# Kernel tuning notes

Hardware: AMD Instinct MI355X
Metric: run time of the kernel (lower is better)

The kernel has to match this reference:

```python
import jax, jax.numpy as jnp
import numpy as np

B, HQ, HKV, D = 32, 32, 8, 128
PAGE_SIZE, PAGES_PER_SEQ = 16, 128
NUM_PAGES = B * PAGES_PER_SEQ
MAX_LEN = PAGE_SIZE * PAGES_PER_SEQ  # 2048
SCALING = 0.08838834764831845  # 1/sqrt(128)
LOGIT_CAP = 50.0


def setup_inputs() -> dict:
    key = jax.random.key(0)
    ks = jax.random.split(key, 6)
    q = jax.random.normal(ks[0], (B, HQ * D), jnp.float32)
    k = jax.random.normal(ks[1], (B, HKV * D), jnp.float32)
    v = jax.random.normal(ks[2], (B, HKV * D), jnp.float32)
    k_cache = jax.random.normal(ks[3], (NUM_PAGES, PAGE_SIZE, HKV, D), jnp.float32)
    v_cache = jax.random.normal(ks[4], (NUM_PAGES, PAGE_SIZE, HKV, D), jnp.float32)
    # disjoint page assignment: request b owns pages [b*128, (b+1)*128)
    page_table = jnp.arange(NUM_PAGES, dtype=jnp.int32).reshape(B, PAGES_PER_SEQ)
    seq_lens = jax.random.randint(ks[5], (B,), 1, MAX_LEN + 1, dtype=jnp.int32)
    return dict(q=q, k=k, v=v, k_cache=k_cache, v_cache=v_cache,
                page_table=page_table, seq_lens=seq_lens)


def reference(q, k, v, k_cache, v_cache, page_table, seq_lens):
    # mirror RadixAttention.forward's k.view(-1, Hkv, D) / v.view(-1, Hkv, D)
    kn = k.reshape(B, HKV, D)
    vn = v.reshape(B, HKV, D)

    # save_kv_cache=True: scatter new token (at position seq_len-1) into paged cache
    pos = seq_lens - 1
    page = page_table[jnp.arange(B), pos // PAGE_SIZE]  # [B]
    slot = pos % PAGE_SIZE                              # [B]
    k_cache = k_cache.at[page, slot].set(kn)
    v_cache = v_cache.at[page, slot].set(vn)

    # gather paged KV per request: [B, Lmax, Hkv, D]
    Kb = k_cache[page_table].reshape(B, MAX_LEN, HKV, D)
    Vb = v_cache[page_table].reshape(B, MAX_LEN, HKV, D)

    # GQA: query head h maps to kv head h // (HQ//HKV)
    G = HQ // HKV
    qh = q.reshape(B, HKV, G, D)
    scores = jnp.einsum('bkgd,blkd->bkgl', qh, Kb) * SCALING  # [B,Hkv,G,L]
    scores = LOGIT_CAP * jnp.tanh(scores / LOGIT_CAP)          # logit capping

    valid = jnp.arange(MAX_LEN, dtype=jnp.int32)[None, :] < seq_lens[:, None]  # [B,L]
    scores = jnp.where(valid[:, None, None, :], scores, -jnp.inf)
    p = jax.nn.softmax(scores, axis=-1)
    out = jnp.einsum('bkgl,blkd->bkgd', p, Vb)  # [B,Hkv,G,D]
    return out.reshape(B, HQ * D)
```

## Files before the change

### kernel.cpp

```cpp
#include <hip/hip_runtime.h>
#include <hip/hip_bf16.h>
#include <math.h>

#define BB 32
#define HQ 32
#define HKV 8
#define DD 128
#define PAGE_SZ 16
#define PAGES_PER_SEQ 128
#define MAX_LEN 2048
#define GG 4
#define NCHUNK 8
#define CHUNK 256
#define SCALING 0.08838834764831845f
#define CAP 50.0f
#define WS_STRIDE 520

__global__ __launch_bounds__(256, 4) void attn_partial(
    const float* __restrict__ q,
    const float* __restrict__ knew,
    const float* __restrict__ vnew,
    const float* __restrict__ k_cache,
    const float* __restrict__ v_cache,
    const int* __restrict__ page_table,
    const int* __restrict__ seq_lens,
    float* __restrict__ ws)
{
    const int idx = blockIdx.x;
    const int c  = idx % NCHUNK;
    const int bh = idx / NCHUNK;
    const int h  = bh % HKV;
    const int b  = bh / HKV;

    const int L  = seq_lens[b];
    const int t0 = c * CHUNK;
    const int t1 = min(t0 + CHUNK, L);
    float* wsb = ws + (size_t)idx * WS_STRIDE;

    if (t0 >= t1) {
        if (threadIdx.x < GG) { wsb[threadIdx.x] = -INFINITY; wsb[GG + threadIdx.x] = 0.0f; }
        return;
    }
    const int NT = t1 - t0;

    __shared__ float s_q[GG][DD];
    __shared__ float s_sc[GG][CHUNK];
    __shared__ float s_red[8][GG * DD];
    __shared__ int   s_pages[CHUNK / PAGE_SZ];
    __shared__ float s_m[GG], s_l[GG];

    const int tid = threadIdx.x;

    for (int i = tid; i < GG * DD; i += 256) {
        int g = i / DD, d = i % DD;
        s_q[g][d] = q[(size_t)b * (HQ * DD) + (h * GG + g) * DD + d];
    }
    if (tid < CHUNK / PAGE_SZ)
        s_pages[tid] = page_table[b * PAGES_PER_SEQ + t0 / PAGE_SZ + tid];
    __syncthreads();

    const int hw = tid >> 5;
    const int ln = tid & 31;

    float4 qf[GG];
    #pragma unroll
    for (int g = 0; g < GG; g++) qf[g] = *(const float4*)&s_q[g][4 * ln];

    const float4* knew_row = (const float4*)&knew[(size_t)b * (HKV * DD) + h * DD];
    const float4* vnew_row = (const float4*)&vnew[(size_t)b * (HKV * DD) + h * DD];

    for (int i = 0; i < CHUNK / 32; i++) {
        const int tbase = t0 + i * 32 + hw;
        if (tbase >= t1) break;

        float4 kv[4];
        int   trel[4];
        bool  vld[4];
        #pragma unroll
        for (int j = 0; j < 4; j++) {
            int t = tbase + j * 8;
            vld[j] = (t < t1);
            int tc = vld[j] ? t : tbase;
            trel[j] = tc - t0;
            const float4* krow;
            if (tc == L - 1) {
                krow = knew_row;
            } else {
                int page = s_pages[trel[j] >> 4];
                int slot = tc & (PAGE_SZ - 1);
                krow = (const float4*)&k_cache[((size_t)page * PAGE_SZ + slot) * (HKV * DD) + h * DD];
            }
            kv[j] = krow[ln];
        }

        float dots[4][GG];
        #pragma unroll
        for (int j = 0; j < 4; j++) {
            #pragma unroll
            for (int g = 0; g < GG; g++)
                dots[j][g] = kv[j].x * qf[g].x + kv[j].y * qf[g].y
                           + kv[j].z * qf[g].z + kv[j].w * qf[g].w;
        }
        #pragma unroll
        for (int m = 1; m < 32; m <<= 1) {
            #pragma unroll
            for (int j = 0; j < 4; j++)
                #pragma unroll
                for (int g = 0; g < GG; g++)
                    dots[j][g] += __shfl_xor(dots[j][g], m);
        }
        if (ln == 0) {
            #pragma unroll
            for (int j = 0; j < 4; j++)
                if (vld[j])
                    #pragma unroll
                    for (int g = 0; g < GG; g++)
                        s_sc[g][trel[j]] = dots[j][g];
        }
    }
    __syncthreads();

    {
        int g  = tid >> 6;
        int wl = tid & 63;
        float mx = -INFINITY;
        for (int t = wl; t < NT; t += 64) {
            float s = s_sc[g][t];
            s = CAP * tanhf(s * (SCALING * (1.0f / CAP)));
            s_sc[g][t] = s;
            mx = fmaxf(mx, s);
        }
        #pragma unroll
        for (int m = 1; m < 64; m <<= 1) mx = fmaxf(mx, __shfl_xor(mx, m));
        float sum = 0.0f;
        for (int t = wl; t < NT; t += 64) {
            float e = __expf(s_sc[g][t] - mx);
            s_sc[g][t] = e;
            sum += e;
        }
        #pragma unroll
        for (int m = 1; m < 64; m <<= 1) sum += __shfl_xor(sum, m);
        if (wl == 0) { s_m[g] = mx; s_l[g] = sum; }
    }
    __syncthreads();

    float4 acc[GG];
    #pragma unroll
    for (int g = 0; g < GG; g++) acc[g] = make_float4(0.f, 0.f, 0.f, 0.f);

    for (int i = 0; i < CHUNK / 32; i++) {
        const int tbase = t0 + i * 32 + hw;
        if (tbase >= t1) break;

        float4 vv[4];
        int   trel[4];
        bool  vld[4];
        #pragma unroll
        for (int j = 0; j < 4; j++) {
            int t = tbase + j * 8;
            vld[j] = (t < t1);
            int tc = vld[j] ? t : tbase;
            trel[j] = tc - t0;
            const float4* vrow;
            if (tc == L - 1) {
                vrow = vnew_row;
            } else {
                int page = s_pages[trel[j] >> 4];
                int slot = tc & (PAGE_SZ - 1);
                vrow = (const float4*)&v_cache[((size_t)page * PAGE_SZ + slot) * (HKV * DD) + h * DD];
            }
            vv[j] = vrow[ln];
        }
        float p[4][GG];
        #pragma unroll
        for (int j = 0; j < 4; j++)
            #pragma unroll
            for (int g = 0; g < GG; g++)
                p[j][g] = vld[j] ? s_sc[g][trel[j]] : 0.0f;

        #pragma unroll
        for (int j = 0; j < 4; j++) {
            #pragma unroll
            for (int g = 0; g < GG; g++) {
                acc[g].x += p[j][g] * vv[j].x; acc[g].y += p[j][g] * vv[j].y;
                acc[g].z += p[j][g] * vv[j].z; acc[g].w += p[j][g] * vv[j].w;
            }
        }
    }
    #pragma unroll
    for (int g = 0; g < GG; g++)
        *(float4*)&s_red[hw][g * DD + 4 * ln] = acc[g];
    __syncthreads();

    for (int i = tid; i < GG * DD; i += 256) {
        float s = 0.f;
        #pragma unroll
        for (int w = 0; w < 8; w++) s += s_red[w][i];
        wsb[8 + i] = s;
    }
    if (tid < GG) { wsb[tid] = s_m[tid]; wsb[GG + tid] = s_l[tid]; }
}

__global__ __launch_bounds__(512) void attn_combine(
    const float* __restrict__ ws, float* __restrict__ out)
{
    const int bh = blockIdx.x;
    const int h  = bh % HKV;
    const int b  = bh / HKV;
    const int tid = threadIdx.x;
    const int g = tid / DD;
    const int d = tid % DD;

    float mv[NCHUNK], lv[NCHUNK];
    float M = -INFINITY;
    #pragma unroll
    for (int c = 0; c < NCHUNK; c++) {
        const float* wsb = ws + (size_t)(bh * NCHUNK + c) * WS_STRIDE;
        mv[c] = wsb[g];
        lv[c] = wsb[GG + g];
        if (lv[c] > 0.0f) M = fmaxf(M, mv[c]);
    }
    float lsum = 0.0f, osum = 0.0f;
    #pragma unroll
    for (int c = 0; c < NCHUNK; c++) {
        if (lv[c] > 0.0f) {
            const float* wsb = ws + (size_t)(bh * NCHUNK + c) * WS_STRIDE;
            float a = __expf(mv[c] - M);
            lsum += lv[c] * a;
            osum += wsb[8 + g * DD + d] * a;
        }
    }
    out[(size_t)b * (HQ * DD) + (h * GG + g) * DD + d] = osum / lsum;
}

extern "C" void kernel_launch(void* const* d_in, const int* in_sizes, int n_in,
                              void* d_out, int out_size, void* d_ws, size_t ws_size,
                              hipStream_t stream) {
    const float* q       = (const float*)d_in[0];
    const float* k       = (const float*)d_in[1];
    const float* v       = (const float*)d_in[2];
    const float* k_cache = (const float*)d_in[3];
    const float* v_cache = (const float*)d_in[4];
    const int* page_table = (const int*)d_in[5];
    const int* seq_lens   = (const int*)d_in[6];
    float* out = (float*)d_out;
    float* ws  = (float*)d_ws;

    attn_partial<<<BB * HKV * NCHUNK, 256, 0, stream>>>(
        q, k, v, k_cache, v_cache, page_table, seq_lens, ws);
    attn_combine<<<BB * HKV, 512, 0, stream>>>(ws, out);
}
```

Before: 482.3 us.

## Restructure QK phase with 8-lane token groups, DPP reductions and prefetch

The QK score loop now maps eight tokens per 64-lane wavefront, with each eight-lane group covering one key row. Dot products are reduced with three DPP row_shr adds instead of a five-step 32-wide shfl_xor reduction over 16 values. The next iteration's K rows are software-prefetched into registers. This cuts cross-lane shuffle traffic and hides load latency, at the cost of more registers (q held as 16 float4). The PV loop's early-exit condition was also changed to be uniform per iteration.

New measurement: 475.9 us. About the same (-1.3%).

```diff
diff --git a/kernel.cpp b/kernel.cpp
--- a/kernel.cpp
+++ b/kernel.cpp
@@ -15,6 +15,17 @@
 #define SCALING 0.08838834764831845f
 #define CAP 50.0f
 #define WS_STRIDE 520
+
+__device__ __forceinline__ float dpp8_sum(float x) {
+    int t;
+    t = __builtin_amdgcn_update_dpp(0, __float_as_int(x), 0x111, 0xF, 0xF, true);
+    x += __int_as_float(t);
+    t = __builtin_amdgcn_update_dpp(0, __float_as_int(x), 0x112, 0xF, 0xF, true);
+    x += __int_as_float(t);
+    t = __builtin_amdgcn_update_dpp(0, __float_as_int(x), 0x114, 0xF, 0xF, true);
+    x += __int_as_float(t);
+    return x;
+}
 
 __global__ __launch_bounds__(256, 4) void attn_partial(
     const float* __restrict__ q,
@@ -59,64 +70,69 @@
         s_pages[tid] = page_table[b * PAGES_PER_SEQ + t0 / PAGE_SZ + tid];
     __syncthreads();
 
-    const int hw = tid >> 5;
-    const int ln = tid & 31;
-
-    float4 qf[GG];
-    #pragma unroll
-    for (int g = 0; g < GG; g++) qf[g] = *(const float4*)&s_q[g][4 * ln];
-
-    const float4* knew_row = (const float4*)&knew[(size_t)b * (HKV * DD) + h * DD];
-    const float4* vnew_row = (const float4*)&vnew[(size_t)b * (HKV * DD) + h * DD];
-
-    for (int i = 0; i < CHUNK / 32; i++) {
-        const int tbase = t0 + i * 32 + hw;
-        if (tbase >= t1) break;
-
-        float4 kv[4];
-        int   trel[4];
-        bool  vld[4];
-        #pragma unroll
-        for (int j = 0; j < 4; j++) {
-            int t = tbase + j * 8;
-            vld[j] = (t < t1);
-            int tc = vld[j] ? t : tbase;
-            trel[j] = tc - t0;
-            const float4* krow;
-            if (tc == L - 1) {
-                krow = knew_row;
-            } else {
-                int page = s_pages[trel[j] >> 4];
-                int slot = tc & (PAGE_SZ - 1);
-                krow = (const float4*)&k_cache[((size_t)page * PAGE_SZ + slot) * (HKV * DD) + h * DD];
-            }
-            kv[j] = krow[ln];
-        }
-
-        float dots[4][GG];
-        #pragma unroll
-        for (int j = 0; j < 4; j++) {
-            #pragma unroll
-            for (int g = 0; g < GG; g++)
-                dots[j][g] = kv[j].x * qf[g].x + kv[j].y * qf[g].y
-                           + kv[j].z * qf[g].z + kv[j].w * qf[g].w;
-        }
-        #pragma unroll
-        for (int m = 1; m < 32; m <<= 1) {
-            #pragma unroll
-            for (int j = 0; j < 4; j++)
+    const float* knew_row = &knew[(size_t)b * (HKV * DD) + h * DD];
+    const float* vnew_row = &vnew[(size_t)b * (HKV * DD) + h * DD];
+
+    {
+        const int wv = tid >> 6;
+        const int ln = tid & 63;
+        const int tg = ln >> 3;
+        const int lg = ln & 7;
+
+        float4 qf[GG][4];
+        #pragma unroll
+        for (int g = 0; g < GG; g++)
+            #pragma unroll
+            for (int p = 0; p < 4; p++)
+                qf[g][p] = *(const float4*)&s_q[g][p * 32 + lg * 4];
+
+        const int niter = (NT + 31) >> 5;
+
+#define LOAD_K(I, KV, WT) do {                                                \
+        int t_ = t0 + (I) * 32 + wv * 8 + tg;                                 \
+        bool vld_ = t_ < t1;                                                  \
+        int tc_ = vld_ ? t_ : (t1 - 1);                                       \
+        const float* row_;                                                    \
+        if (tc_ == L - 1) row_ = knew_row;                                    \
+        else {                                                                \
+            int page_ = s_pages[(tc_ - t0) >> 4];                             \
+            int slot_ = tc_ & (PAGE_SZ - 1);                                  \
+            row_ = &k_cache[((size_t)page_ * PAGE_SZ + slot_) * (HKV * DD) + h * DD]; \
+        }                                                                     \
+        const float4* r4_ = (const float4*)row_;                              \
+        KV[0] = r4_[lg]; KV[1] = r4_[8 + lg];                                 \
+        KV[2] = r4_[16 + lg]; KV[3] = r4_[24 + lg];                           \
+        WT = vld_ ? (t_ - t0) : -1;                                           \
+    } while (0)
+
+        float4 kva[4];
+        int wta;
+        LOAD_K(0, kva, wta);
+
+        for (int i = 0; i < niter; i++) {
+            float4 kvb[4];
+            int wtb = -1;
+            if (i + 1 < niter) LOAD_K(i + 1, kvb, wtb);
+
+            float dots[GG];
+            #pragma unroll
+            for (int g = 0; g < GG; g++) {
+                float s = 0.0f;
                 #pragma unroll
-                for (int g = 0; g < GG; g++)
-                    dots[j][g] += __shfl_xor(dots[j][g], m);
-        }
-        if (ln == 0) {
-            #pragma unroll
-            for (int j = 0; j < 4; j++)
-                if (vld[j])
-                    #pragma unroll
-                    for (int g = 0; g < GG; g++)
-                        s_sc[g][trel[j]] = dots[j][g];
-        }
+                for (int p = 0; p < 4; p++)
+                    s += kva[p].x * qf[g][p].x + kva[p].y * qf[g][p].y
+                       + kva[p].z * qf[g][p].z + kva[p].w * qf[g][p].w;
+                dots[g] = dpp8_sum(s);
+            }
+            if (lg == 7 && wta >= 0) {
+                #pragma unroll
+                for (int g = 0; g < GG; g++) s_sc[g][wta] = dots[g];
+            }
+            #pragma unroll
+            for (int p = 0; p < 4; p++) kva[p] = kvb[p];
+            wta = wtb;
+        }
+#undef LOAD_K
     }
     __syncthreads();
 
@@ -144,13 +160,16 @@
     }
     __syncthreads();
 
+    const int hw = tid >> 5;
+    const int ln = tid & 31;
+
     float4 acc[GG];
     #pragma unroll
     for (int g = 0; g < GG; g++) acc[g] = make_float4(0.f, 0.f, 0.f, 0.f);
 
     for (int i = 0; i < CHUNK / 32; i++) {
         const int tbase = t0 + i * 32 + hw;
-        if (tbase >= t1) break;
+        if (t0 + i * 32 >= t1) break;
 
         float4 vv[4];
         int   trel[4];
@@ -163,7 +182,7 @@
             trel[j] = tc - t0;
             const float4* vrow;
             if (tc == L - 1) {
-                vrow = vnew_row;
+                vrow = (const float4*)vnew_row;
             } else {
                 int page = s_pages[trel[j] >> 4];
                 int slot = tc & (PAGE_SZ - 1);
```
